# Kernel optimization log

Hardware: AMD Instinct MI355X
Metric: run time of the kernel (lower is better)

The kernel has to match this reference:

```python
import jax, jax.numpy as jnp
import numpy as np

STATE = 128
B = 32768
H = 8  # attention heads, head_dim = 64
EPS = 1e-5

@jax.custom_vjp
def spike(u):
    # Heaviside spike with snntorch ATan surrogate (alpha=2)
    return (u > 0).astype(u.dtype)

def _spike_fwd(u):
    return spike(u), u

def _spike_bwd(u, g):
    return (g / (1.0 + (jnp.pi * u) ** 2),)

spike.defvjp(_spike_fwd, _spike_bwd)

def _ln(x, g, b):
    m = jnp.mean(x, axis=-1, keepdims=True)
    v = jnp.var(x, axis=-1, keepdims=True)
    return (x - m) * jax.lax.rsqrt(v + EPS) * g + b

def _lrelu(x):
    return jnp.where(x >= 0, x, 0.1 * x)

def _lif(mem, x, beta, thr):
    # snntorch Leaky, reset_mechanism='zero': reset from previous mem (detached)
    reset = jax.lax.stop_gradient((mem > thr).astype(mem.dtype))
    mem = (beta * mem + x) * (1.0 - reset)
    spk = spike(mem - thr)
    return spk, mem

def _p(k, shape, fan_in):
    return jax.random.normal(k, shape, jnp.float32) * (fan_in ** -0.5)

def setup_inputs():
    key = jax.random.key(0)
    ks = list(jax.random.split(key, 16))
    nk = iter(ks).__next__
    inp = {}
    inp['x'] = jax.random.normal(nk(), (B, STATE), jnp.float32)
    inp['g_in'] = jnp.ones((STATE,), jnp.float32); inp['b_in'] = jnp.zeros((STATE,), jnp.float32)
    inp['W_vis'] = _p(nk(), (STATE, 512), STATE); inp['b_vis'] = jnp.zeros((512,), jnp.float32)
    inp['g_vis'] = jnp.ones((512,), jnp.float32); inp['bg_vis'] = jnp.zeros((512,), jnp.float32)
    inp['W_qkv'] = _p(nk(), (512, 1536), 512); inp['b_qkv'] = jnp.zeros((1536,), jnp.float32)
    inp['W_o'] = _p(nk(), (512, 512), 512); inp['b_o'] = jnp.zeros((512,), jnp.float32)
    inp['W1'] = _p(nk(), (512, 256), 512); inp['b1'] = jnp.zeros((256,), jnp.float32)
    inp['g1'] = jnp.ones((256,), jnp.float32); inp['bg1'] = jnp.zeros((256,), jnp.float32)
    inp['W2'] = _p(nk(), (256, 128), 256); inp['b2'] = jnp.zeros((128,), jnp.float32)
    inp['g2'] = jnp.ones((128,), jnp.float32); inp['bg2'] = jnp.zeros((128,), jnp.float32)
    inp['W3'] = _p(nk(), (128, 64), 128); inp['b3'] = jnp.zeros((64,), jnp.float32)
    inp['g3'] = jnp.ones((64,), jnp.float32); inp['bg3'] = jnp.zeros((64,), jnp.float32)
    inp['Ws0'] = _p(nk(), (64, 64), 64); inp['bs0'] = jnp.zeros((64,), jnp.float32)
    inp['Ws1'] = _p(nk(), (64, 64), 64); inp['bs1'] = jnp.zeros((64,), jnp.float32)
    inp['Ws2'] = _p(nk(), (64, 32), 64); inp['bs2'] = jnp.zeros((32,), jnp.float32)
    inp['Ws3'] = _p(nk(), (32, 32), 32); inp['bs3'] = jnp.zeros((32,), jnp.float32)
    inp['W_out'] = _p(nk(), (32, 5), 32); inp['b_out'] = jnp.zeros((5,), jnp.float32)
    inp['time_window'] = 10
    return inp

def _forward(x, g_in, b_in, W_vis, b_vis, g_vis, bg_vis, W_qkv, b_qkv, W_o, b_o,
             W1, b1, g1, bg1, W2, b2, g2, bg2, W3, b3, g3, bg3,
             Ws0, bs0, Ws1, bs1, Ws2, bs2, Ws3, bs3, W_out, b_out, time_window):
    n = x.shape[0]
    x = _ln(x, g_in, b_in)
    vis = _ln(_lrelu(x @ W_vis + b_vis), g_vis, bg_vis)  # dropout = identity (eval)
    # MultiheadAttention on seq_len=1: softmax over a single key is exactly 1,
    # so attn_out = out_proj(v_proj(vis)). Keep q/k projections for fidelity of math flow.
    qkv = vis @ W_qkv + b_qkv
    v = qkv[:, 1024:]
    attn = v @ W_o + b_o  # [n, 512]
    res1 = _ln(_lrelu(attn @ W1 + b1), g1, bg1) + attn[:, :256]
    res2 = _ln(_lrelu(res1 @ W2 + b2), g2, bg2) + res1[:, :128]
    res3 = _ln(_lrelu(res2 @ W3 + b3), g3, bg3) + res2[:, :64]

    x0 = res3 @ Ws0 + bs0  # constant across time steps (input to lif0 each step)

    def step(carry, _):
        m0, m1, m2, m3, acc = carry
        s0, m0 = _lif(m0, x0, 0.95, 0.8)
        s1, m1 = _lif(m1, s0 @ Ws1 + bs1, 0.92, 0.85)
        s2, m2 = _lif(m2, s1 @ Ws2 + bs2, 0.90, 0.90)
        s3, m3 = _lif(m3, s2 @ Ws3 + bs3, 0.85, 0.95)
        acc = acc + jax.nn.sigmoid(s3 @ W_out + b_out)
        return (m0, m1, m2, m3, acc), None

    z = lambda d: jnp.zeros((n, d), x.dtype)
    init = (z(64), z(64), z(32), z(32), z(5))
    (_, _, _, _, spikes), _ = jax.lax.scan(step, init, None, length=time_window)
    return spikes / time_window

def reference(x, g_in, b_in, W_vis, b_vis, g_vis, bg_vis, W_qkv, b_qkv, W_o, b_o,
              W1, b1, g1, bg1, W2, b2, g2, bg2, W3, b3, g3, bg3,
              Ws0, bs0, Ws1, bs1, Ws2, bs2, Ws3, bs3, W_out, b_out, time_window):
    return _forward(x, g_in, b_in, W_vis, b_vis, g_vis, bg_vis, W_qkv, b_qkv, W_o, b_o,
                    W1, b1, g1, bg1, W2, b2, g2, bg2, W3, b3, g3, bg3,
                    Ws0, bs0, Ws1, bs1, Ws2, bs2, Ws3, bs3, W_out, b_out, time_window)
```

## Files before the change

### kernel.cpp

```cpp
#include <hip/hip_runtime.h>


template<int W, bool HASRES>
__global__ __launch_bounds__(256) void ln_np(const float* in, float* out,
        const float* g, const float* b, const float* res, int resStride, int rows)
{
    constexpr int E = W / 64;
    __shared__ float lds[4][W];
    int wave = threadIdx.x >> 6, lane = threadIdx.x & 63;
    int row = blockIdx.x * 4 + wave;
    const float* rp = in + (size_t)row * W;
    float v[E];
    #pragma unroll
    for (int e = 0; e < E; ++e) {
        v[e] = rp[e * 64 + lane];
        lds[wave][e * 64 + lane] = v[e];
    }
    __syncthreads();

    auto reduce_np = [&](const float* p) -> float {
        if constexpr (W == 64) {
            int j = lane & 7;
            float r = p[j];
            #pragma unroll
            for (int i = 8; i < 64; i += 8) r = __fadd_rn(r, p[i + j]);
            r = __fadd_rn(r, __shfl_xor(r, 1));
            r = __fadd_rn(r, __shfl_xor(r, 2));
            r = __fadd_rn(r, __shfl_xor(r, 4));
            return r;
        } else {
            constexpr int NB = W / 128;
            int grp = (lane >> 4) % NB;
            int sub = lane & 15;
            const float* q = p + grp * 128 + sub;
            float t = __fadd_rn(
                __fadd_rn(__fadd_rn(q[0],  q[16]), __fadd_rn(q[32], q[48])),
                __fadd_rn(__fadd_rn(q[64], q[80]), __fadd_rn(q[96], q[112])));
            t = __fadd_rn(t, __shfl_xor(t, 8));
            t = __fadd_rn(t, __shfl_xor(t, 4));
            t = __fadd_rn(t, __shfl_xor(t, 2));
            t = __fadd_rn(t, __shfl_xor(t, 1));
            if constexpr (NB >= 2) t = __fadd_rn(t, __shfl_xor(t, 16));
            if constexpr (NB == 4) t = __fadd_rn(t, __shfl_xor(t, 32));
            return t;
        }
    };

    float m = __fdiv_rn(reduce_np(lds[wave]), (float)W);
    __syncthreads();
    #pragma unroll
    for (int e = 0; e < E; ++e) {
        float d = __fsub_rn(v[e], m);
        lds[wave][e * 64 + lane] = __fmul_rn(d, d);
    }
    __syncthreads();
    float var = __fdiv_rn(reduce_np(lds[wave]), (float)W);
    float vpe = __fadd_rn(var, 1e-5f);
    float rs  = __fdiv_rn(1.0f, __fsqrt_rn(vpe));
    float* op = out + (size_t)row * W;
    #pragma unroll
    for (int e = 0; e < E; ++e) {
        int c = e * 64 + lane;
        float o = __fadd_rn(__fmul_rn(__fmul_rn(__fsub_rn(v[e], m), rs), g[c]), b[c]);
        if (HASRES) o = __fadd_rn(o, res[(size_t)row * resStride + c]);
        op[c] = o;
    }
}

template<int K, int TN, int SPLIT, bool LRELU>
__global__ __launch_bounds__(256) void gemm2(const float* A, const float* Wt,
        const float* bias, float* out, int ldb, int colOff, int nOut)
{
    constexpr int CPT = TN / 16;
    constexpr bool TWO = (SPLIT < K);
    __shared__ __align__(16) float As[32 * 132];
    __shared__ __align__(16) float Bs[32 * TN];
    int tid = threadIdx.x;
    int rg = tid >> 4;
    int cg = tid & 15;
    int rowBase = blockIdx.x * 128;
    int colTile = blockIdx.y * TN;

    float acc1[8][CPT];
    float acc2[TWO ? 8 : 1][TWO ? CPT : 1];
    #pragma unroll
    for (int r = 0; r < 8; ++r)
        #pragma unroll
        for (int c = 0; c < CPT; ++c) acc1[r][c] = 0.f;
    if constexpr (TWO) {
        #pragma unroll
        for (int r = 0; r < 8; ++r)
            #pragma unroll
            for (int c = 0; c < CPT; ++c) acc2[r][c] = 0.f;
    }

    for (int kc = 0; kc < K; kc += 32) {
        {
            int row = tid >> 1, koff = (tid & 1) * 16;
            const float* ap = &A[(size_t)(rowBase + row) * K + kc + koff];
            #pragma unroll
            for (int j = 0; j < 4; ++j) {
                const float4 v4 = *reinterpret_cast<const float4*>(ap + 4 * j);
                As[(koff + 4 * j + 0) * 132 + row] = v4.x;
                As[(koff + 4 * j + 1) * 132 + row] = v4.y;
                As[(koff + 4 * j + 2) * 132 + row] = v4.z;
                As[(koff + 4 * j + 3) * 132 + row] = v4.w;
            }
        }
        constexpr int NF4 = (32 * TN / 4) / 256;
        #pragma unroll
        for (int j = 0; j < NF4; ++j) {
            int i = tid + j * 256;
            int k = i / (TN / 4), c4 = i % (TN / 4);
            *reinterpret_cast<float4*>(&Bs[k * TN + c4 * 4]) =
                *reinterpret_cast<const float4*>(
                    &Wt[(size_t)(kc + k) * ldb + colOff + colTile + c4 * 4]);
        }
        __syncthreads();
        bool hi = TWO && (kc >= SPLIT);
        #pragma unroll
        for (int k = 0; k < 32; ++k) {
            float a[8];
            const float4 a0 = *reinterpret_cast<const float4*>(&As[k * 132 + rg * 8]);
            const float4 a1 = *reinterpret_cast<const float4*>(&As[k * 132 + rg * 8 + 4]);
            a[0] = a0.x; a[1] = a0.y; a[2] = a0.z; a[3] = a0.w;
            a[4] = a1.x; a[5] = a1.y; a[6] = a1.z; a[7] = a1.w;
            float bv[CPT];
            const float4 b0 = *reinterpret_cast<const float4*>(&Bs[k * TN + cg * CPT]);
            bv[0] = b0.x; bv[1] = b0.y; bv[2] = b0.z; bv[3] = b0.w;
            if constexpr (CPT == 8) {
                const float4 b1 = *reinterpret_cast<const float4*>(&Bs[k * TN + cg * CPT + 4]);
                bv[4] = b1.x; bv[5] = b1.y; bv[6] = b1.z; bv[7] = b1.w;
            }
            if (!hi) {
                #pragma unroll
                for (int r = 0; r < 8; ++r)
                    #pragma unroll
                    for (int c = 0; c < CPT; ++c)
                        acc1[r][c] = __fmaf_rn(a[r], bv[c], acc1[r][c]);
            } else {
                #pragma unroll
                for (int r = 0; r < 8; ++r)
                    #pragma unroll
                    for (int c = 0; c < CPT; ++c)
                        acc2[r][c] = __fmaf_rn(a[r], bv[c], acc2[r][c]);
            }
        }
        __syncthreads();
    }
    #pragma unroll
    for (int r = 0; r < 8; ++r) {
        int row = rowBase + rg * 8 + r;
        float res[CPT];
        #pragma unroll
        for (int c = 0; c < CPT; ++c) {
            float t = acc1[r][c];
            if constexpr (TWO) t = __fadd_rn(t, acc2[r][c]);
            float v = __fadd_rn(t, bias[colTile + cg * CPT + c]);
            if (LRELU) v = (v >= 0.f) ? v : __fmul_rn(0.1f, v);
            res[c] = v;
        }
        float* orow = &out[(size_t)row * nOut + colTile + cg * CPT];
        *reinterpret_cast<float4*>(orow) = make_float4(res[0], res[1], res[2], res[3]);
        if constexpr (CPT == 8)
            *reinterpret_cast<float4*>(orow + 4) = make_float4(res[4], res[5], res[6], res[7]);
    }
}

__device__ void run_pair(float x0, float biasA, float biasB,
    int T, int lane, int l32, int l5,
    const float* lWs1, const float* lWs2, const float* lWs3, const float* lWout,
    const float* lbs1, const float* lbs2, const float* lbs3, const float* lbout,
    float& dA, float& dB, bool& eq)
{
    float tA0 = 0.8f + biasA, tA1 = 0.85f + biasA, tA2 = 0.9f + biasA, tA3 = 0.95f + biasA;
    float tB0 = 0.8f + biasB, tB1 = 0.85f + biasB, tB2 = 0.9f + biasB, tB3 = 0.95f + biasB;
    float mA0 = 0.f, mA1 = 0.f, mA2 = 0.f, mA3 = 0.f, accA = 0.f;
    float mB0 = 0.f, mB1 = 0.f, mB2 = 0.f, mB3 = 0.f, accB = 0.f;
    bool same = true;
    unsigned long long pA3 = ~0ull, pB3 = ~0ull;
    float sgA = 0.f, sgB = 0.f;
    for (int t = 0; t < T; ++t) {
        bool r;
        r = mA0 > tA0; mA0 = r ? 0.f : __fadd_rn(__fmul_rn(0.95f, mA0), x0);
        r = mB0 > tB0; mB0 = r ? 0.f : __fadd_rn(__fmul_rn(0.95f, mB0), x0);
        unsigned long long kA = __ballot(mA0 > tA0);
        unsigned long long kB = __ballot(mB0 > tB0);
        same = same && (kA == kB);
        float hA = 0.f, hB = 0.f;
        #pragma unroll
        for (int i = 0; i < 64; ++i) {
            float w = lWs1[i * 64 + lane];
            hA = __fmaf_rn((float)(int)((kA >> i) & 1), w, hA);
            hB = __fmaf_rn((float)(int)((kB >> i) & 1), w, hB);
        }
        hA = __fadd_rn(hA, lbs1[lane]);
        hB = __fadd_rn(hB, lbs1[lane]);
        r = mA1 > tA1; mA1 = r ? 0.f : __fadd_rn(__fmul_rn(0.92f, mA1), hA);
        r = mB1 > tB1; mB1 = r ? 0.f : __fadd_rn(__fmul_rn(0.92f, mB1), hB);
        kA = __ballot(mA1 > tA1);
        kB = __ballot(mB1 > tB1);
        same = same && (kA == kB);
        hA = 0.f; hB = 0.f;
        #pragma unroll
        for (int i = 0; i < 64; ++i) {
            float w = lWs2[i * 32 + l32];
            hA = __fmaf_rn((float)(int)((kA >> i) & 1), w, hA);
            hB = __fmaf_rn((float)(int)((kB >> i) & 1), w, hB);
        }
        hA = __fadd_rn(hA, lbs2[l32]);
        hB = __fadd_rn(hB, lbs2[l32]);
        r = mA2 > tA2; mA2 = r ? 0.f : __fadd_rn(__fmul_rn(0.9f, mA2), hA);
        r = mB2 > tB2; mB2 = r ? 0.f : __fadd_rn(__fmul_rn(0.9f, mB2), hB);
        kA = __ballot(mA2 > tA2) & 0xffffffffull;
        kB = __ballot(mB2 > tB2) & 0xffffffffull;
        same = same && (kA == kB);
        hA = 0.f; hB = 0.f;
        #pragma unroll
        for (int i = 0; i < 32; ++i) {
            float w = lWs3[i * 32 + l32];
            hA = __fmaf_rn((float)(int)((kA >> i) & 1), w, hA);
            hB = __fmaf_rn((float)(int)((kB >> i) & 1), w, hB);
        }
        hA = __fadd_rn(hA, lbs3[l32]);
        hB = __fadd_rn(hB, lbs3[l32]);
        r = mA3 > tA3; mA3 = r ? 0.f : __fadd_rn(__fmul_rn(0.85f, mA3), hA);
        r = mB3 > tB3; mB3 = r ? 0.f : __fadd_rn(__fmul_rn(0.85f, mB3), hB);
        kA = __ballot(mA3 > tA3) & 0xffffffffull;
        kB = __ballot(mB3 > tB3) & 0xffffffffull;
        same = same && (kA == kB);
        if (kA != pA3) {
            float o = 0.f;
            #pragma unroll
            for (int i = 0; i < 32; ++i)
                o = __fmaf_rn((float)(int)((kA >> i) & 1), lWout[i * 5 + l5], o);
            o = __fadd_rn(o, lbout[l5]);
            sgA = (float)(1.0 / (1.0 + exp(-(double)o)));
            pA3 = kA;
        }
        if (kB != pB3) {
            float o = 0.f;
            #pragma unroll
            for (int i = 0; i < 32; ++i)
                o = __fmaf_rn((float)(int)((kB >> i) & 1), lWout[i * 5 + l5], o);
            o = __fadd_rn(o, lbout[l5]);
            sgB = (float)(1.0 / (1.0 + exp(-(double)o)));
            pB3 = kB;
        }
        accA = __fadd_rn(accA, sgA);
        accB = __fadd_rn(accB, sgB);
    }
    dA = __fdiv_rn(accA, (float)T);
    dB = __fdiv_rn(accB, (float)T);
    eq = same;
}

__global__ __launch_bounds__(256) void snn2(const float* x0buf,
    const float* Ws1, const float* bs1,
    const float* Ws2, const float* bs2,
    const float* Ws3, const float* bs3,
    const float* Wout, const float* bout,
    const int* twp, float* out, int rows)
{
    __shared__ float lWs1[4096], lWs2[2048], lWs3[1024], lWout[160];
    __shared__ float lbs1[64], lbs2[32], lbs3[32], lbout[8];
    int tid = threadIdx.x;
    for (int i = tid; i < 4096; i += 256) lWs1[i] = Ws1[i];
    for (int i = tid; i < 2048; i += 256) lWs2[i] = Ws2[i];
    for (int i = tid; i < 1024; i += 256) lWs3[i] = Ws3[i];
    for (int i = tid; i < 160;  i += 256) lWout[i] = Wout[i];
    if (tid < 64) lbs1[tid] = bs1[tid];
    if (tid < 32) { lbs2[tid] = bs2[tid]; lbs3[tid] = bs3[tid]; }
    if (tid < 5)  lbout[tid] = bout[tid];
    __syncthreads();
    const int T = *twp;
    int lane = tid & 63;
    int l32  = lane & 31;
    int l5   = (lane < 5) ? lane : 0;
    const float EPS3 = 4e-6f / 3.0f;
    const float bA = -3.0f * EPS3, bB = 3.0f * EPS3;
    const float tA0 = 0.8f + bA, tA1 = 0.85f + bA, tA2 = 0.9f + bA, tA3 = 0.95f + bA;
    const float tB0 = 0.8f + bB, tB1 = 0.85f + bB, tB2 = 0.9f + bB, tB3 = 0.95f + bB;
    int wid = blockIdx.x * 4 + (tid >> 6);
    int nw = gridDim.x * 4;
    int npair = rows >> 1;
    for (int p = wid; p < npair; p += nw) {
        int rP = p * 2, rQ = rP + 1;
        float xP = x0buf[(size_t)rP * 64 + lane];
        float xQ = x0buf[(size_t)rQ * 64 + lane];
        float mP0 = 0.f, mP1 = 0.f, mP2 = 0.f, mP3 = 0.f, accP = 0.f;
        float mQ0 = 0.f, mQ1 = 0.f, mQ2 = 0.f, mQ3 = 0.f, accQ = 0.f;
        bool okP = true, okQ = true;
        unsigned long long pk3P = ~0ull, pk3Q = ~0ull;
        float sgP = 0.f, sgQ = 0.f;
        for (int t = 0; t < T; ++t) {
            bool r;
            r = mP0 > tA0; mP0 = r ? 0.f : __fadd_rn(__fmul_rn(0.95f, mP0), xP);
            r = mQ0 > tA0; mQ0 = r ? 0.f : __fadd_rn(__fmul_rn(0.95f, mQ0), xQ);
            unsigned long long kP = __ballot(mP0 > tA0);
            unsigned long long kQ = __ballot(mQ0 > tA0);
            okP = okP && (kP == __ballot(mP0 > tB0));
            okQ = okQ && (kQ == __ballot(mQ0 > tB0));
            float hP = 0.f, hQ = 0.f;
            {
                unsigned int loP = (unsigned int)kP, hiP = (unsigned int)(kP >> 32);
                unsigned int loQ = (unsigned int)kQ, hiQ = (unsigned int)(kQ >> 32);
                #pragma unroll
                for (int i = 0; i < 32; ++i) {
                    float w = lWs1[i * 64 + lane];
                    hP = __fmaf_rn((float)((loP >> i) & 1u), w, hP);
                    hQ = __fmaf_rn((float)((loQ >> i) & 1u), w, hQ);
                }
                #pragma unroll
                for (int i = 0; i < 32; ++i) {
                    float w = lWs1[(i + 32) * 64 + lane];
                    hP = __fmaf_rn((float)((hiP >> i) & 1u), w, hP);
                    hQ = __fmaf_rn((float)((hiQ >> i) & 1u), w, hQ);
                }
            }
            hP = __fadd_rn(hP, lbs1[lane]);
            hQ = __fadd_rn(hQ, lbs1[lane]);
            r = mP1 > tA1; mP1 = r ? 0.f : __fadd_rn(__fmul_rn(0.92f, mP1), hP);
            r = mQ1 > tA1; mQ1 = r ? 0.f : __fadd_rn(__fmul_rn(0.92f, mQ1), hQ);
            kP = __ballot(mP1 > tA1);
            kQ = __ballot(mQ1 > tA1);
            okP = okP && (kP == __ballot(mP1 > tB1));
            okQ = okQ && (kQ == __ballot(mQ1 > tB1));
            hP = 0.f; hQ = 0.f;
            {
                unsigned int loP = (unsigned int)kP, hiP = (unsigned int)(kP >> 32);
                unsigned int loQ = (unsigned int)kQ, hiQ = (unsigned int)(kQ >> 32);
                #pragma unroll
                for (int i = 0; i < 32; ++i) {
                    float w = lWs2[i * 32 + l32];
                    hP = __fmaf_rn((float)((loP >> i) & 1u), w, hP);
                    hQ = __fmaf_rn((float)((loQ >> i) & 1u), w, hQ);
                }
                #pragma unroll
                for (int i = 0; i < 32; ++i) {
                    float w = lWs2[(i + 32) * 32 + l32];
                    hP = __fmaf_rn((float)((hiP >> i) & 1u), w, hP);
                    hQ = __fmaf_rn((float)((hiQ >> i) & 1u), w, hQ);
                }
            }
            hP = __fadd_rn(hP, lbs2[l32]);
            hQ = __fadd_rn(hQ, lbs2[l32]);
            r = mP2 > tA2; mP2 = r ? 0.f : __fadd_rn(__fmul_rn(0.9f, mP2), hP);
            r = mQ2 > tA2; mQ2 = r ? 0.f : __fadd_rn(__fmul_rn(0.9f, mQ2), hQ);
            kP = __ballot(mP2 > tA2) & 0xffffffffull;
            kQ = __ballot(mQ2 > tA2) & 0xffffffffull;
            okP = okP && (kP == (__ballot(mP2 > tB2) & 0xffffffffull));
            okQ = okQ && (kQ == (__ballot(mQ2 > tB2) & 0xffffffffull));
            hP = 0.f; hQ = 0.f;
            {
                unsigned int loP = (unsigned int)kP;
                unsigned int loQ = (unsigned int)kQ;
                #pragma unroll
                for (int i = 0; i < 32; ++i) {
                    float w = lWs3[i * 32 + l32];
                    hP = __fmaf_rn((float)((loP >> i) & 1u), w, hP);
                    hQ = __fmaf_rn((float)((loQ >> i) & 1u), w, hQ);
                }
            }
            hP = __fadd_rn(hP, lbs3[l32]);
            hQ = __fadd_rn(hQ, lbs3[l32]);
            r = mP3 > tA3; mP3 = r ? 0.f : __fadd_rn(__fmul_rn(0.85f, mP3), hP);
            r = mQ3 > tA3; mQ3 = r ? 0.f : __fadd_rn(__fmul_rn(0.85f, mQ3), hQ);
            kP = __ballot(mP3 > tA3) & 0xffffffffull;
            kQ = __ballot(mQ3 > tA3) & 0xffffffffull;
            okP = okP && (kP == (__ballot(mP3 > tB3) & 0xffffffffull));
            okQ = okQ && (kQ == (__ballot(mQ3 > tB3) & 0xffffffffull));
            if (kP != pk3P) {
                float o = 0.f;
                unsigned int lo = (unsigned int)kP;
                #pragma unroll
                for (int i = 0; i < 32; ++i)
                    o = __fmaf_rn((float)((lo >> i) & 1u), lWout[i * 5 + l5], o);
                o = __fadd_rn(o, lbout[l5]);
                sgP = (float)(1.0 / (1.0 + exp(-(double)o)));
                pk3P = kP;
            }
            if (kQ != pk3Q) {
                float o = 0.f;
                unsigned int lo = (unsigned int)kQ;
                #pragma unroll
                for (int i = 0; i < 32; ++i)
                    o = __fmaf_rn((float)((lo >> i) & 1u), lWout[i * 5 + l5], o);
                o = __fadd_rn(o, lbout[l5]);
                sgQ = (float)(1.0 / (1.0 + exp(-(double)o)));
                pk3Q = kQ;
            }
            accP = __fadd_rn(accP, sgP);
            accQ = __fadd_rn(accQ, sgQ);
        }
        float dP = __fdiv_rn(accP, (float)T);
        float dQ = __fdiv_rn(accQ, (float)T);
        float osumP, osumQ;
        if (okP) {
            osumP = dP + dP; osumP = osumP + dP; osumP = osumP + dP;
        } else {
            float d0, d3, d1, d2; bool e;
            run_pair(xP, -3.0f * EPS3, 3.0f * EPS3, T, lane, l32, l5,
                     lWs1, lWs2, lWs3, lWout, lbs1, lbs2, lbs3, lbout, d0, d3, e);
            run_pair(xP, -1.0f * EPS3, 1.0f * EPS3, T, lane, l32, l5,
                     lWs1, lWs2, lWs3, lWout, lbs1, lbs2, lbs3, lbout, d1, d2, e);
            osumP = d0 + d1; osumP = osumP + d2; osumP = osumP + d3;
        }
        if (okQ) {
            osumQ = dQ + dQ; osumQ = osumQ + dQ; osumQ = osumQ + dQ;
        } else {
            float d0, d3, d1, d2; bool e;
            run_pair(xQ, -3.0f * EPS3, 3.0f * EPS3, T, lane, l32, l5,
                     lWs1, lWs2, lWs3, lWout, lbs1, lbs2, lbs3, lbout, d0, d3, e);
            run_pair(xQ, -1.0f * EPS3, 1.0f * EPS3, T, lane, l32, l5,
                     lWs1, lWs2, lWs3, lWout, lbs1, lbs2, lbs3, lbout, d1, d2, e);
            osumQ = d0 + d1; osumQ = osumQ + d2; osumQ = osumQ + d3;
        }
        if (lane < 5) {
            out[(size_t)rP * 5 + lane] = 0.25f * osumP;
            out[(size_t)rQ * 5 + lane] = 0.25f * osumQ;
        }
    }
}

extern "C" void kernel_launch(void* const* d_in, const int* in_sizes, int n_in,
                              void* d_out, int out_size, void* d_ws, size_t ws_size,
                              hipStream_t stream)
{
    (void)n_in; (void)out_size;
    const float* x      = (const float*)d_in[0];
    const float* g_in   = (const float*)d_in[1];
    const float* b_in   = (const float*)d_in[2];
    const float* W_vis  = (const float*)d_in[3];
    const float* b_vis  = (const float*)d_in[4];
    const float* g_vis  = (const float*)d_in[5];
    const float* bg_vis = (const float*)d_in[6];
    const float* W_qkv  = (const float*)d_in[7];
    const float* b_qkv  = (const float*)d_in[8];
    const float* W_o    = (const float*)d_in[9];
    const float* b_o    = (const float*)d_in[10];
    const float* W1     = (const float*)d_in[11];
    const float* b1     = (const float*)d_in[12];
    const float* g1     = (const float*)d_in[13];
    const float* bg1    = (const float*)d_in[14];
    const float* W2     = (const float*)d_in[15];
    const float* b2     = (const float*)d_in[16];
    const float* g2     = (const float*)d_in[17];
    const float* bg2    = (const float*)d_in[18];
    const float* W3     = (const float*)d_in[19];
    const float* b3     = (const float*)d_in[20];
    const float* g3     = (const float*)d_in[21];
    const float* bg3    = (const float*)d_in[22];
    const float* Ws0    = (const float*)d_in[23];
    const float* bs0    = (const float*)d_in[24];
    const float* Ws1    = (const float*)d_in[25];
    const float* bs1    = (const float*)d_in[26];
    const float* Ws2    = (const float*)d_in[27];
    const float* bs2    = (const float*)d_in[28];
    const float* Ws3    = (const float*)d_in[29];
    const float* bs3    = (const float*)d_in[30];
    const float* Wout   = (const float*)d_in[31];
    const float* bout   = (const float*)d_in[32];
    const int*   twp    = (const int*)d_in[33];
    float* out = (float*)d_out;
    float* ws  = (float*)d_ws;

    const int BROWS = in_sizes[0] / 128;

    const size_t perRowB = 1280 * 4;
    size_t maxRows = ws_size / perRowB;
    if (maxRows > (size_t)BROWS) maxRows = BROWS;
    int Rch = (int)(maxRows & ~(size_t)127);
    if (Rch <= 0) return;

    for (int r0 = 0; r0 < BROWS; r0 += Rch) {
        int rows = (BROWS - r0 < Rch) ? (BROWS - r0) : Rch;
        float* rA = ws;
        float* rB = rA + (size_t)Rch * 512;
        float* rC = rB + (size_t)Rch * 512;
        dim3 blk(256);
        int rb = rows / 4;
        int gx = rows / 128;

        hipLaunchKernelGGL((ln_np<128,false>), dim3(rb), blk, 0, stream,
                           x + (size_t)r0 * 128, rC, g_in, b_in, nullptr, 0, rows);
        hipLaunchKernelGGL((gemm2<128,128,128,true>), dim3(gx,4), blk, 0, stream,
                           rC, W_vis, b_vis, rA, 512, 0, 512);
        hipLaunchKernelGGL((ln_np<512,false>), dim3(rb), blk, 0, stream,
                           rA, rB, g_vis, bg_vis, nullptr, 0, rows);
        hipLaunchKernelGGL((gemm2<512,128,384,false>), dim3(gx,4), blk, 0, stream,
                           rB, W_qkv, b_qkv + 1024, rA, 1536, 1024, 512);
        hipLaunchKernelGGL((gemm2<512,128,384,false>), dim3(gx,4), blk, 0, stream,
                           rA, W_o, b_o, rB, 512, 0, 512);
        hipLaunchKernelGGL((gemm2<512,128,384,true>), dim3(gx,2), blk, 0, stream,
                           rB, W1, b1, rC, 256, 0, 256);
        hipLaunchKernelGGL((ln_np<256,true>), dim3(rb), blk, 0, stream,
                           rC, rA, g1, bg1, rB, 512, rows);
        hipLaunchKernelGGL((gemm2<256,128,256,true>), dim3(gx,1), blk, 0, stream,
                           rA, W2, b2, rB, 128, 0, 128);
        hipLaunchKernelGGL((ln_np<128,true>), dim3(rb), blk, 0, stream,
                           rB, rC, g2, bg2, rA, 256, rows);
        hipLaunchKernelGGL((gemm2<128,64,128,true>), dim3(gx,1), blk, 0, stream,
                           rC, W3, b3, rA, 64, 0, 64);
        hipLaunchKernelGGL((ln_np<64,true>), dim3(rb), blk, 0, stream,
                           rA, rB, g3, bg3, rC, 128, rows);
        hipLaunchKernelGGL((gemm2<64,64,64,false>), dim3(gx,1), blk, 0, stream,
                           rB, Ws0, bs0, rA, 64, 0, 64);
        hipLaunchKernelGGL(snn2, dim3(2048), blk, 0, stream,
                           rA, Ws1, bs1, Ws2, bs2, Ws3, bs3,
                           Wout, bout, twp, out + (size_t)r0 * 5, rows);
    }
}
```

Before: 1.584 ms.

## Register-prefetch GEMM tiles, batch four rows per SNN wave, defer fallback rows

The GEMM kernel now loads the next K-chunk of A and B into registers while the current chunk is being computed, which hides global load latency. The SNN kernel processes four rows per wave instead of two. It reads transposed, XOR-swizzled weights from LDS as float4 vectors. Rows whose spikes are ambiguous near the threshold are no longer re-simulated inline, which made the wave diverge; they go onto an atomic fail list that a separate small kernel processes. The cost is higher register pressure, an extra memset and kernel launch, and a workspace reservation for the fail list.

Result: slower. 1.720 ms (+8.6%).

```diff
diff --git a/kernel.cpp b/kernel.cpp
--- a/kernel.cpp
+++ b/kernel.cpp
@@ -73,6 +73,7 @@
 {
     constexpr int CPT = TN / 16;
     constexpr bool TWO = (SPLIT < K);
+    constexpr int NF4 = (32 * TN / 4) / 256;
     __shared__ __align__(16) float As[32 * 132];
     __shared__ __align__(16) float Bs[32 * TN];
     int tid = threadIdx.x;
@@ -80,6 +81,20 @@
     int cg = tid & 15;
     int rowBase = blockIdx.x * 128;
     int colTile = blockIdx.y * TN;
+    int arow = tid >> 1, akoff = (tid & 1) * 16;
+    const float* aBase = &A[(size_t)(rowBase + arow) * K + akoff];
+    const float* bBase = &Wt[colOff + colTile];
+
+    float4 pa[4], pb[NF4];
+    #pragma unroll
+    for (int j = 0; j < 4; ++j)
+        pa[j] = *reinterpret_cast<const float4*>(aBase + 4 * j);
+    #pragma unroll
+    for (int j = 0; j < NF4; ++j) {
+        int i = tid + j * 256;
+        int k = i / (TN / 4), c4 = i % (TN / 4);
+        pb[j] = *reinterpret_cast<const float4*>(&bBase[(size_t)k * ldb + c4 * 4]);
+    }
 
     float acc1[8][CPT];
     float acc2[TWO ? 8 : 1][TWO ? CPT : 1];
@@ -95,28 +110,32 @@
     }
 
     for (int kc = 0; kc < K; kc += 32) {
-        {
-            int row = tid >> 1, koff = (tid & 1) * 16;
-            const float* ap = &A[(size_t)(rowBase + row) * K + kc + koff];
-            #pragma unroll
-            for (int j = 0; j < 4; ++j) {
-                const float4 v4 = *reinterpret_cast<const float4*>(ap + 4 * j);
-                As[(koff + 4 * j + 0) * 132 + row] = v4.x;
-                As[(koff + 4 * j + 1) * 132 + row] = v4.y;
-                As[(koff + 4 * j + 2) * 132 + row] = v4.z;
-                As[(koff + 4 * j + 3) * 132 + row] = v4.w;
-            }
-        }
-        constexpr int NF4 = (32 * TN / 4) / 256;
+        #pragma unroll
+        for (int j = 0; j < 4; ++j) {
+            As[(akoff + 4 * j + 0) * 132 + arow] = pa[j].x;
+            As[(akoff + 4 * j + 1) * 132 + arow] = pa[j].y;
+            As[(akoff + 4 * j + 2) * 132 + arow] = pa[j].z;
+            As[(akoff + 4 * j + 3) * 132 + arow] = pa[j].w;
+        }
         #pragma unroll
         for (int j = 0; j < NF4; ++j) {
             int i = tid + j * 256;
             int k = i / (TN / 4), c4 = i % (TN / 4);
-            *reinterpret_cast<float4*>(&Bs[k * TN + c4 * 4]) =
-                *reinterpret_cast<const float4*>(
-                    &Wt[(size_t)(kc + k) * ldb + colOff + colTile + c4 * 4]);
+            *reinterpret_cast<float4*>(&Bs[k * TN + c4 * 4]) = pb[j];
         }
         __syncthreads();
+        if (kc + 32 < K) {
+            #pragma unroll
+            for (int j = 0; j < 4; ++j)
+                pa[j] = *reinterpret_cast<const float4*>(aBase + kc + 32 + 4 * j);
+            #pragma unroll
+            for (int j = 0; j < NF4; ++j) {
+                int i = tid + j * 256;
+                int k = i / (TN / 4), c4 = i % (TN / 4);
+                pb[j] = *reinterpret_cast<const float4*>(
+                    &bBase[(size_t)(kc + 32 + k) * ldb + c4 * 4]);
+            }
+        }
         bool hi = TWO && (kc >= SPLIT);
         #pragma unroll
         for (int k = 0; k < 32; ++k) {
@@ -255,12 +274,191 @@
     eq = same;
 }
 
-__global__ __launch_bounds__(256) void snn2(const float* x0buf,
+__global__ __launch_bounds__(256) void snn3(const float* x0buf,
     const float* Ws1, const float* bs1,
     const float* Ws2, const float* bs2,
     const float* Ws3, const float* bs3,
     const float* Wout, const float* bout,
-    const int* twp, float* out, int rows)
+    const int* twp, float* out, int rows, int* faillist)
+{
+    __shared__ __align__(16) float w1T[4096], w2T[2048], w3T[1024], woT[160];
+    __shared__ float lbs1[64], lbs2[32], lbs3[32], lbout[8];
+    int tid = threadIdx.x;
+    for (int e = tid; e < 4096; e += 256) {
+        int l = e & 63, i = e >> 6;
+        w1T[l * 64 + (i ^ ((l & 7) << 2))] = Ws1[e];
+    }
+    for (int e = tid; e < 2048; e += 256) {
+        int l = e & 31, i = e >> 5;
+        w2T[l * 64 + (i ^ ((l & 7) << 2))] = Ws2[e];
+    }
+    for (int e = tid; e < 1024; e += 256) {
+        int l = e & 31, i = e >> 5;
+        w3T[l * 32 + (i ^ ((l & 7) << 2))] = Ws3[e];
+    }
+    for (int e = tid; e < 160; e += 256) {
+        int l = e % 5, i = e / 5;
+        woT[l * 32 + (i ^ ((l & 7) << 2))] = Wout[e];
+    }
+    if (tid < 64) lbs1[tid] = bs1[tid];
+    if (tid < 32) { lbs2[tid] = bs2[tid]; lbs3[tid] = bs3[tid]; }
+    if (tid < 5)  lbout[tid] = bout[tid];
+    __syncthreads();
+    const int T = *twp;
+    int lane = tid & 63;
+    int l32  = lane & 31;
+    int l5   = (lane < 5) ? lane : 0;
+    int swz  = (lane & 7) << 2;
+    int swz32 = (l32 & 7) << 2;
+    int swz5  = (l5 & 7) << 2;
+    const float EPS3 = 4e-6f / 3.0f;
+    const float bA = -3.0f * EPS3, bB = 3.0f * EPS3;
+    const float tA0 = 0.8f + bA, tA1 = 0.85f + bA, tA2 = 0.9f + bA, tA3 = 0.95f + bA;
+    const float tB0 = 0.8f + bB, tB1 = 0.85f + bB, tB2 = 0.9f + bB, tB3 = 0.95f + bB;
+    int wid = blockIdx.x * 4 + (tid >> 6);
+    int nw = gridDim.x * 4;
+    int nquad = rows >> 2;
+    for (int q = wid; q < nquad; q += nw) {
+        int rowb = q * 4;
+        float x[4], m0[4], m1[4], m2[4], m3[4], acc[4], sg[4];
+        unsigned long long pk3[4];
+        bool ok[4];
+        #pragma unroll
+        for (int r = 0; r < 4; ++r) {
+            x[r] = x0buf[(size_t)(rowb + r) * 64 + lane];
+            m0[r] = 0.f; m1[r] = 0.f; m2[r] = 0.f; m3[r] = 0.f;
+            acc[r] = 0.f; sg[r] = 0.f; pk3[r] = ~0ull; ok[r] = true;
+        }
+        for (int t = 0; t < T; ++t) {
+            unsigned long long k0[4];
+            #pragma unroll
+            for (int r = 0; r < 4; ++r) {
+                bool rr = m0[r] > tA0;
+                m0[r] = rr ? 0.f : __fadd_rn(__fmul_rn(0.95f, m0[r]), x[r]);
+                k0[r] = __ballot(m0[r] > tA0);
+                ok[r] = ok[r] && (k0[r] == __ballot(m0[r] > tB0));
+            }
+            float h[4] = {0.f, 0.f, 0.f, 0.f};
+            unsigned lo[4], hi[4];
+            #pragma unroll
+            for (int r = 0; r < 4; ++r) { lo[r] = (unsigned)k0[r]; hi[r] = (unsigned)(k0[r] >> 32); }
+            #pragma unroll
+            for (int i0 = 0; i0 < 64; i0 += 4) {
+                const float4 wv = *reinterpret_cast<const float4*>(&w1T[lane * 64 + (i0 ^ swz)]);
+                #pragma unroll
+                for (int j = 0; j < 4; ++j) {
+                    const int i = i0 + j;
+                    const float w = (i == i0) ? wv.x : (i == i0 + 1) ? wv.y : (i == i0 + 2) ? wv.z : wv.w;
+                    #pragma unroll
+                    for (int r = 0; r < 4; ++r) {
+                        unsigned bits = (i < 32) ? lo[r] : hi[r];
+                        float mf = ((bits >> (i & 31)) & 1u) ? 1.0f : 0.0f;
+                        h[r] = __fmaf_rn(mf, w, h[r]);
+                    }
+                }
+            }
+            unsigned long long k1[4];
+            #pragma unroll
+            for (int r = 0; r < 4; ++r) {
+                h[r] = __fadd_rn(h[r], lbs1[lane]);
+                bool rr = m1[r] > tA1;
+                m1[r] = rr ? 0.f : __fadd_rn(__fmul_rn(0.92f, m1[r]), h[r]);
+                k1[r] = __ballot(m1[r] > tA1);
+                ok[r] = ok[r] && (k1[r] == __ballot(m1[r] > tB1));
+            }
+            #pragma unroll
+            for (int r = 0; r < 4; ++r) { h[r] = 0.f; lo[r] = (unsigned)k1[r]; hi[r] = (unsigned)(k1[r] >> 32); }
+            #pragma unroll
+            for (int i0 = 0; i0 < 64; i0 += 4) {
+                const float4 wv = *reinterpret_cast<const float4*>(&w2T[l32 * 64 + (i0 ^ swz32)]);
+                #pragma unroll
+                for (int j = 0; j < 4; ++j) {
+                    const int i = i0 + j;
+                    const float w = (i == i0) ? wv.x : (i == i0 + 1) ? wv.y : (i == i0 + 2) ? wv.z : wv.w;
+                    #pragma unroll
+                    for (int r = 0; r < 4; ++r) {
+                        unsigned bits = (i < 32) ? lo[r] : hi[r];
+                        float mf = ((bits >> (i & 31)) & 1u) ? 1.0f : 0.0f;
+                        h[r] = __fmaf_rn(mf, w, h[r]);
+                    }
+                }
+            }
+            unsigned k2[4];
+            #pragma unroll
+            for (int r = 0; r < 4; ++r) {
+                h[r] = __fadd_rn(h[r], lbs2[l32]);
+                bool rr = m2[r] > tA2;
+                m2[r] = rr ? 0.f : __fadd_rn(__fmul_rn(0.9f, m2[r]), h[r]);
+                k2[r] = (unsigned)(__ballot(m2[r] > tA2) & 0xffffffffull);
+                ok[r] = ok[r] && (k2[r] == (unsigned)(__ballot(m2[r] > tB2) & 0xffffffffull));
+            }
+            #pragma unroll
+            for (int r = 0; r < 4; ++r) h[r] = 0.f;
+            #pragma unroll
+            for (int i0 = 0; i0 < 32; i0 += 4) {
+                const float4 wv = *reinterpret_cast<const float4*>(&w3T[l32 * 32 + (i0 ^ swz32)]);
+                #pragma unroll
+                for (int j = 0; j < 4; ++j) {
+                    const int i = i0 + j;
+                    const float w = (i == i0) ? wv.x : (i == i0 + 1) ? wv.y : (i == i0 + 2) ? wv.z : wv.w;
+                    #pragma unroll
+                    for (int r = 0; r < 4; ++r) {
+                        float mf = ((k2[r] >> i) & 1u) ? 1.0f : 0.0f;
+                        h[r] = __fmaf_rn(mf, w, h[r]);
+                    }
+                }
+            }
+            unsigned long long k3[4];
+            #pragma unroll
+            for (int r = 0; r < 4; ++r) {
+                h[r] = __fadd_rn(h[r], lbs3[l32]);
+                bool rr = m3[r] > tA3;
+                m3[r] = rr ? 0.f : __fadd_rn(__fmul_rn(0.85f, m3[r]), h[r]);
+                k3[r] = __ballot(m3[r] > tA3) & 0xffffffffull;
+                ok[r] = ok[r] && (k3[r] == (__ballot(m3[r] > tB3) & 0xffffffffull));
+            }
+            #pragma unroll
+            for (int r = 0; r < 4; ++r) {
+                if (k3[r] != pk3[r]) {
+                    float o = 0.f;
+                    unsigned kk = (unsigned)k3[r];
+                    #pragma unroll
+                    for (int i0 = 0; i0 < 32; i0 += 4) {
+                        const float4 wv = *reinterpret_cast<const float4*>(&woT[l5 * 32 + (i0 ^ swz5)]);
+                        #pragma unroll
+                        for (int j = 0; j < 4; ++j) {
+                            const int i = i0 + j;
+                            const float w = (i == i0) ? wv.x : (i == i0 + 1) ? wv.y : (i == i0 + 2) ? wv.z : wv.w;
+                            float mf = ((kk >> i) & 1u) ? 1.0f : 0.0f;
+                            o = __fmaf_rn(mf, w, o);
+                        }
+                    }
+                    o = __fadd_rn(o, lbout[l5]);
+                    sg[r] = (float)(1.0 / (1.0 + exp(-(double)o)));
+                    pk3[r] = k3[r];
+                }
+                acc[r] = __fadd_rn(acc[r], sg[r]);
+            }
+        }
+        #pragma unroll
+        for (int r = 0; r < 4; ++r) {
+            float d = __fdiv_rn(acc[r], (float)T);
+            float osum = d + d; osum = osum + d; osum = osum + d;
+            if (lane < 5) out[(size_t)(rowb + r) * 5 + lane] = 0.25f * osum;
+            if (!ok[r] && lane == 0) {
+                int idx = atomicAdd(&faillist[0], 1);
+                faillist[1 + idx] = rowb + r;
+            }
+        }
+    }
+}
+
+__global__ __launch_bounds__(256) void snn_slow(const float* x0buf,
+    const float* Ws1, const float* bs1,
+    const float* Ws2, const float* bs2,
+    const float* Ws3, const float* bs3,
+    const float* Wout, const float* bout,
+    const int* twp, float* out, const int* faillist)
 {
     __shared__ float lWs1[4096], lWs2[2048], lWs3[1024], lWout[160];
     __shared__ float lbs1[64], lbs2[32], lbs3[32], lbout[8];
@@ -278,148 +476,19 @@
     int l32  = lane & 31;
     int l5   = (lane < 5) ? lane : 0;
     const float EPS3 = 4e-6f / 3.0f;
-    const float bA = -3.0f * EPS3, bB = 3.0f * EPS3;
-    const float tA0 = 0.8f + bA, tA1 = 0.85f + bA, tA2 = 0.9f + bA, tA3 = 0.95f + bA;
-    const float tB0 = 0.8f + bB, tB1 = 0.85f + bB, tB2 = 0.9f + bB, tB3 = 0.95f + bB;
+    int nf = faillist[0];
     int wid = blockIdx.x * 4 + (tid >> 6);
     int nw = gridDim.x * 4;
-    int npair = rows >> 1;
-    for (int p = wid; p < npair; p += nw) {
-        int rP = p * 2, rQ = rP + 1;
-        float xP = x0buf[(size_t)rP * 64 + lane];
-        float xQ = x0buf[(size_t)rQ * 64 + lane];
-        float mP0 = 0.f, mP1 = 0.f, mP2 = 0.f, mP3 = 0.f, accP = 0.f;
-        float mQ0 = 0.f, mQ1 = 0.f, mQ2 = 0.f, mQ3 = 0.f, accQ = 0.f;
-        bool okP = true, okQ = true;
-        unsigned long long pk3P = ~0ull, pk3Q = ~0ull;
-        float sgP = 0.f, sgQ = 0.f;
-        for (int t = 0; t < T; ++t) {
-            bool r;
-            r = mP0 > tA0; mP0 = r ? 0.f : __fadd_rn(__fmul_rn(0.95f, mP0), xP);
-            r = mQ0 > tA0; mQ0 = r ? 0.f : __fadd_rn(__fmul_rn(0.95f, mQ0), xQ);
-            unsigned long long kP = __ballot(mP0 > tA0);
-            unsigned long long kQ = __ballot(mQ0 > tA0);
-            okP = okP && (kP == __ballot(mP0 > tB0));
-            okQ = okQ && (kQ == __ballot(mQ0 > tB0));
-            float hP = 0.f, hQ = 0.f;
-            {
-                unsigned int loP = (unsigned int)kP, hiP = (unsigned int)(kP >> 32);
-                unsigned int loQ = (unsigned int)kQ, hiQ = (unsigned int)(kQ >> 32);
-                #pragma unroll
-                for (int i = 0; i < 32; ++i) {
-                    float w = lWs1[i * 64 + lane];
-                    hP = __fmaf_rn((float)((loP >> i) & 1u), w, hP);
-                    hQ = __fmaf_rn((float)((loQ >> i) & 1u), w, hQ);
-                }
-                #pragma unroll
-                for (int i = 0; i < 32; ++i) {
-                    float w = lWs1[(i + 32) * 64 + lane];
-                    hP = __fmaf_rn((float)((hiP >> i) & 1u), w, hP);
-                    hQ = __fmaf_rn((float)((hiQ >> i) & 1u), w, hQ);
-                }
-            }
-            hP = __fadd_rn(hP, lbs1[lane]);
-            hQ = __fadd_rn(hQ, lbs1[lane]);
-            r = mP1 > tA1; mP1 = r ? 0.f : __fadd_rn(__fmul_rn(0.92f, mP1), hP);
-            r = mQ1 > tA1; mQ1 = r ? 0.f : __fadd_rn(__fmul_rn(0.92f, mQ1), hQ);
-            kP = __ballot(mP1 > tA1);
-            kQ = __ballot(mQ1 > tA1);
-            okP = okP && (kP == __ballot(mP1 > tB1));
-            okQ = okQ && (kQ == __ballot(mQ1 > tB1));
-            hP = 0.f; hQ = 0.f;
-            {
-                unsigned int loP = (unsigned int)kP, hiP = (unsigned int)(kP >> 32);
-                unsigned int loQ = (unsigned int)kQ, hiQ = (unsigned int)(kQ >> 32);
-                #pragma unroll
-                for (int i = 0; i < 32; ++i) {
-                    float w = lWs2[i * 32 + l32];
-                    hP = __fmaf_rn((float)((loP >> i) & 1u), w, hP);
-                    hQ = __fmaf_rn((float)((loQ >> i) & 1u), w, hQ);
-                }
-                #pragma unroll
-                for (int i = 0; i < 32; ++i) {
-                    float w = lWs2[(i + 32) * 32 + l32];
-                    hP = __fmaf_rn((float)((hiP >> i) & 1u), w, hP);
-                    hQ = __fmaf_rn((float)((hiQ >> i) & 1u), w, hQ);
-                }
-            }
-            hP = __fadd_rn(hP, lbs2[l32]);
-            hQ = __fadd_rn(hQ, lbs2[l32]);
-            r = mP2 > tA2; mP2 = r ? 0.f : __fadd_rn(__fmul_rn(0.9f, mP2), hP);
-            r = mQ2 > tA2; mQ2 = r ? 0.f : __fadd_rn(__fmul_rn(0.9f, mQ2), hQ);
-            kP = __ballot(mP2 > tA2) & 0xffffffffull;
-            kQ = __ballot(mQ2 > tA2) & 0xffffffffull;
-            okP = okP && (kP == (__ballot(mP2 > tB2) & 0xffffffffull));
-            okQ = okQ && (kQ == (__ballot(mQ2 > tB2) & 0xffffffffull));
-            hP = 0.f; hQ = 0.f;
-            {
-                unsigned int loP = (unsigned int)kP;
-                unsigned int loQ = (unsigned int)kQ;
-                #pragma unroll
-                for (int i = 0; i < 32; ++i) {
-                    float w = lWs3[i * 32 + l32];
-                    hP = __fmaf_rn((float)((loP >> i) & 1u), w, hP);
-                    hQ = __fmaf_rn((float)((loQ >> i) & 1u), w, hQ);
-                }
-            }
-            hP = __fadd_rn(hP, lbs3[l32]);
-            hQ = __fadd_rn(hQ, lbs3[l32]);
-            r = mP3 > tA3; mP3 = r ? 0.f : __fadd_rn(__fmul_rn(0.85f, mP3), hP);
-            r = mQ3 > tA3; mQ3 = r ? 0.f : __fadd_rn(__fmul_rn(0.85f, mQ3), hQ);
-            kP = __ballot(mP3 > tA3) & 0xffffffffull;
-            kQ = __ballot(mQ3 > tA3) & 0xffffffffull;
-            okP = okP && (kP == (__ballot(mP3 > tB3) & 0xffffffffull));
-            okQ = okQ && (kQ == (__ballot(mQ3 > tB3) & 0xffffffffull));
-            if (kP != pk3P) {
-                float o = 0.f;
-                unsigned int lo = (unsigned int)kP;
-                #pragma unroll
-                for (int i = 0; i < 32; ++i)
-                    o = __fmaf_rn((float)((lo >> i) & 1u), lWout[i * 5 + l5], o);
-                o = __fadd_rn(o, lbout[l5]);
-                sgP = (float)(1.0 / (1.0 + exp(-(double)o)));
-                pk3P = kP;
-            }
-            if (kQ != pk3Q) {
-                float o = 0.f;
-                unsigned int lo = (unsigned int)kQ;
-                #pragma unroll
-                for (int i = 0; i < 32; ++i)
-                    o = __fmaf_rn((float)((lo >> i) & 1u), lWout[i * 5 + l5], o);
-                o = __fadd_rn(o, lbout[l5]);
-                sgQ = (float)(1.0 / (1.0 + exp(-(double)o)));
-                pk3Q = kQ;
-            }
-            accP = __fadd_rn(accP, sgP);
-            accQ = __fadd_rn(accQ, sgQ);
-        }
-        float dP = __fdiv_rn(accP, (float)T);
-        float dQ = __fdiv_rn(accQ, (float)T);
-        float osumP, osumQ;
-        if (okP) {
-            osumP = dP + dP; osumP = osumP + dP; osumP = osumP + dP;
-        } else {
-            float d0, d3, d1, d2; bool e;
-            run_pair(xP, -3.0f * EPS3, 3.0f * EPS3, T, lane, l32, l5,
-                     lWs1, lWs2, lWs3, lWout, lbs1, lbs2, lbs3, lbout, d0, d3, e);
-            run_pair(xP, -1.0f * EPS3, 1.0f * EPS3, T, lane, l32, l5,
-                     lWs1, lWs2, lWs3, lWout, lbs1, lbs2, lbs3, lbout, d1, d2, e);
-            osumP = d0 + d1; osumP = osumP + d2; osumP = osumP + d3;
-        }
-        if (okQ) {
-            osumQ = dQ + dQ; osumQ = osumQ + dQ; osumQ = osumQ + dQ;
-        } else {
-            float d0, d3, d1, d2; bool e;
-            run_pair(xQ, -3.0f * EPS3, 3.0f * EPS3, T, lane, l32, l5,
-                     lWs1, lWs2, lWs3, lWout, lbs1, lbs2, lbs3, lbout, d0, d3, e);
-            run_pair(xQ, -1.0f * EPS3, 1.0f * EPS3, T, lane, l32, l5,
-                     lWs1, lWs2, lWs3, lWout, lbs1, lbs2, lbs3, lbout, d1, d2, e);
-            osumQ = d0 + d1; osumQ = osumQ + d2; osumQ = osumQ + d3;
-        }
-        if (lane < 5) {
-            out[(size_t)rP * 5 + lane] = 0.25f * osumP;
-            out[(size_t)rQ * 5 + lane] = 0.25f * osumQ;
-        }
+    for (int fi = wid; fi < nf; fi += nw) {
+        int row = faillist[1 + fi];
+        float xR = x0buf[(size_t)row * 64 + lane];
+        float d0, d3, d1, d2; bool e;
+        run_pair(xR, -3.0f * EPS3, 3.0f * EPS3, T, lane, l32, l5,
+                 lWs1, lWs2, lWs3, lWout, lbs1, lbs2, lbs3, lbout, d0, d3, e);
+        run_pair(xR, -1.0f * EPS3, 1.0f * EPS3, T, lane, l32, l5,
+                 lWs1, lWs2, lWs3, lWout, lbs1, lbs2, lbs3, lbout, d1, d2, e);
+        float osum = d0 + d1; osum = osum + d2; osum = osum + d3;
+        if (lane < 5) out[(size_t)row * 5 + lane] = 0.25f * osum;
     }
 }
 
@@ -468,7 +537,9 @@
     const int BROWS = in_sizes[0] / 128;
 
     const size_t perRowB = 1280 * 4;
-    size_t maxRows = ws_size / perRowB;
+    const size_t RES = ((size_t)BROWS + 4) * 4;
+    size_t avail = (ws_size > RES) ? (ws_size - RES) : 0;
+    size_t maxRows = avail / perRowB;
     if (maxRows > (size_t)BROWS) maxRows = BROWS;
     int Rch = (int)(maxRows & ~(size_t)127);
     if (Rch <= 0) return;
@@ -478,6 +549,7 @@
         float* rA = ws;
         float* rB = rA + (size_t)Rch * 512;
         float* rC = rB + (size_t)Rch * 512;
+        int* fail = (int*)(rC + (size_t)Rch * 256);
         dim3 blk(256);
         int rb = rows / 4;
         int gx = rows / 128;
@@ -506,8 +578,12 @@
                            rA, rB, g3, bg3, rC, 128, rows);
         hipLaunchKernelGGL((gemm2<64,64,64,false>), dim3(gx,1), blk, 0, stream,
                            rB, Ws0, bs0, rA, 64, 0, 64);
-        hipLaunchKernelGGL(snn2, dim3(2048), blk, 0, stream,
+        hipMemsetAsync(fail, 0, 4, stream);
+        hipLaunchKernelGGL(snn3, dim3(2048), blk, 0, stream,
                            rA, Ws1, bs1, Ws2, bs2, Ws3, bs3,
-                           Wout, bout, twp, out + (size_t)r0 * 5, rows);
+                           Wout, bout, twp, out + (size_t)r0 * 5, rows, fail);
+        hipLaunchKernelGGL(snn_slow, dim3(64), blk, 0, stream,
+                           rA, Ws1, bs1, Ws2, bs2, Ws3, bs3,
+                           Wout, bout, twp, out + (size_t)r0 * 5, fail);
     }
 }
```
